# Performance work log

Hardware: AMD Instinct MI355X
Metric: run time of the kernel (lower is better)

## Reference

```python
import jax, jax.numpy as jnp
import numpy as np

K = 20  # max_similar_relations


def setup_inputs() -> dict:
    key = jax.random.key(0)
    k1, k2 = jax.random.split(key)
    B, R, D = 256, 2048, 64
    x = jax.random.normal(k1, (B, R, D), dtype=jnp.float32)
    query_rels = jax.random.randint(k2, (B,), 0, R, dtype=jnp.int32)
    return {
        "x": x,
        "query_rels": query_rels,
        # raw params as in __init__: threshold_init=0.2 -> raw=0.2*2-1=-0.6; strength_init=0.05 -> raw=0.05*5-1=-0.75
        "threshold_raw": jnp.float32(-0.6),
        "strength_raw": jnp.float32(-0.75),
        "weight_scale": jnp.float32(1.0),
        "temperature": jnp.float32(1.0),
    }


def reference(x, query_rels, threshold_raw, strength_raw, weight_scale, temperature):
    B, R, D = x.shape
    bidx = jnp.arange(B)
    threshold = jax.nn.sigmoid(threshold_raw)
    strength = jax.nn.sigmoid(strength_raw) * 0.2
    temp = jnp.clip(temperature, 0.1, 10.0)

    # F.normalize(x, p=2, dim=2)
    norms = x / jnp.maximum(jnp.linalg.norm(x, axis=2, keepdims=True), 1e-12)

    q = norms[bidx, query_rels]                      # [B, D] normalized query reprs
    sims = jnp.einsum("bd,brd->br", q, norms)        # [B, R] cosine similarities
    sims = sims.at[bidx, query_rels].set(-1.0)       # exclude self
    sim_w = jax.nn.sigmoid((sims - threshold) * 10.0)

    topv, topi = jax.lax.top_k(sims, K)              # [B, K]
    valid = (topv > threshold) & (topi != query_rels[:, None])

    # softmax over valid top-k entries only (per batch row)
    logits = jnp.where(valid, topv / temp, -1e9)
    w = jax.nn.softmax(logits, axis=1)
    w = jnp.where(valid, w, 0.0)

    sw = jnp.take_along_axis(sim_w, topi, axis=1)    # smooth sigmoid weights of selected
    combined = w * sw
    adjusted = combined * (1.0 + weight_scale * topv)
    adjusted = adjusted / (jnp.sum(adjusted, axis=1, keepdims=True) + 1e-8)

    # gather top-k normalized reprs and weighted-sum them
    top_reprs = jnp.take_along_axis(norms, jnp.broadcast_to(topi[:, :, None], (B, K, D)), axis=1)
    weighted = jnp.einsum("bk,bkd->bd", adjusted, top_reprs)  # [B, D]

    q_orig = x[bidx, query_rels]                     # original (unnormalized) query repr
    has_valid = jnp.any(valid, axis=1, keepdims=True)
    mixed = (1.0 - strength) * q_orig + strength * weighted
    new_q = jnp.where(has_valid, mixed, q_orig)

    return x.at[bidx, query_rels].set(new_q)
```

## Files before the change

### kernel.cpp

```cpp
#include <hip/hip_runtime.h>
#include <math.h>

#define KTOP 20
#define R_MAX 2048

__global__ __launch_bounds__(1024) void fused_enhancer(
    const float* __restrict__ x,
    const int* __restrict__ qrels,
    const float* __restrict__ thr_raw,
    const float* __restrict__ str_raw,
    const float* __restrict__ wscale_p,
    const float* __restrict__ temp_p,
    float* __restrict__ out, int R)
{
    __shared__ float s_q[64];
    __shared__ float s_sims[R_MAX];
    __shared__ float s_dn[R_MAX];
    __shared__ int   s_cand[R_MAX];
    __shared__ int   s_ncand;
    __shared__ float s_topv[KTOP];
    __shared__ int   s_topi[KTOP];
    __shared__ float s_adj[KTOP];
    __shared__ float s_strength;

    const int b = blockIdx.x;
    const int t = threadIdx.x;
    const int qr = qrels[b];
    const float threshold = 1.0f / (1.0f + expf(-thr_raw[0]));

    if (t == 0) s_ncand = 0;

    if (t < 64) {
        float v = x[((long)b * R + qr) * 64 + t];
        float ss = v * v;
#pragma unroll
        for (int m = 1; m < 64; m <<= 1) ss += __shfl_xor(ss, m, 64);
        s_q[t] = v / fmaxf(sqrtf(ss), 1e-12f);
    }
    __syncthreads();

    const int grp = t >> 4, l16 = t & 15;
    const float4 q4 = *(const float4*)(s_q + l16 * 4);
    const long xbase = (long)b * R * 64;
    for (int row = grp; row < R; row += 64) {
        long base = xbase + (long)row * 64 + l16 * 4;
        const float4 v = *(const float4*)(x + base);
        *(float4*)(out + base) = v;
        float dot = v.x * q4.x + v.y * q4.y + v.z * q4.z + v.w * q4.w;
        float ss  = v.x * v.x + v.y * v.y + v.z * v.z + v.w * v.w;
#pragma unroll
        for (int m = 1; m < 16; m <<= 1) {
            dot += __shfl_xor(dot, m, 64);
            ss  += __shfl_xor(ss,  m, 64);
        }
        if (l16 == 0) {
            float dn  = fmaxf(sqrtf(ss), 1e-12f);
            float sim = (row == qr) ? -1.0f : dot / dn;
            s_sims[row] = sim;
            s_dn[row]   = dn;
            if (sim > threshold) {
                int p = atomicAdd(&s_ncand, 1);
                s_cand[p] = row;
            }
        }
    }
    __syncthreads();

    const int ncand = s_ncand;
    const int ksel = ncand < KTOP ? ncand : KTOP;

    if (t < 64) {
        if (ncand > KTOP) {
            float lv[32]; int li[32];
#pragma unroll
            for (int j = 0; j < 32; ++j) {
                int i = t + 64 * j;
                if (i < ncand) { li[j] = s_cand[i]; lv[j] = s_sims[li[j]]; }
                else           { li[j] = 0x7fffffff; lv[j] = -INFINITY; }
            }
            for (int k = 0; k < KTOP; ++k) {
                float bv = -INFINITY; int bi = 0x7fffffff;
#pragma unroll
                for (int j = 0; j < 32; ++j) {
                    if (lv[j] > bv || (lv[j] == bv && li[j] < bi)) { bv = lv[j]; bi = li[j]; }
                }
#pragma unroll
                for (int m = 1; m < 64; m <<= 1) {
                    float v2 = __shfl_xor(bv, m, 64);
                    int   i2 = __shfl_xor(bi, m, 64);
                    if (v2 > bv || (v2 == bv && i2 < bi)) { bv = v2; bi = i2; }
                }
#pragma unroll
                for (int j = 0; j < 32; ++j) if (li[j] == bi) lv[j] = -INFINITY;
                if (t == 0) { s_topv[k] = bv; s_topi[k] = bi; }
            }
        } else if (t == 0) {
            for (int k = 0; k < ksel; ++k) {
                int idx = s_cand[k];
                s_topi[k] = idx;
                s_topv[k] = s_sims[idx];
            }
        }
    }

    if (t == 0) {
        float strength = (1.0f / (1.0f + expf(-str_raw[0]))) * 0.2f;
        float temp = fminf(fmaxf(temp_p[0], 0.1f), 10.0f);
        float wsc  = wscale_p[0];
        if (ksel > 0) {
            float m = -INFINITY;
            for (int k = 0; k < ksel; ++k) m = fmaxf(m, s_topv[k] / temp);
            float w[KTOP]; float wsum = 0.0f;
            for (int k = 0; k < ksel; ++k) { w[k] = expf(s_topv[k] / temp - m); wsum += w[k]; }
            float adj[KTOP]; float asum = 0.0f;
            for (int k = 0; k < ksel; ++k) {
                float tv = s_topv[k];
                float sw = 1.0f / (1.0f + expf(-(tv - threshold) * 10.0f));
                float a  = (w[k] / wsum) * sw * (1.0f + wsc * tv);
                adj[k] = a; asum += a;
            }
            for (int k = 0; k < ksel; ++k)
                s_adj[k] = (adj[k] / (asum + 1e-8f)) / s_dn[s_topi[k]];
        }
        s_strength = strength;
    }
    __syncthreads();

    if (t < 64 && ksel > 0) {
        long qb = ((long)b * R + qr) * 64 + t;
        float qo = x[qb];
        float acc = 0.0f;
        for (int k = 0; k < ksel; ++k)
            acc += s_adj[k] * x[((long)b * R + s_topi[k]) * 64 + t];
        float st = s_strength;
        out[qb] = (1.0f - st) * qo + st * acc;
    }
}

extern "C" void kernel_launch(void* const* d_in, const int* in_sizes, int n_in,
                              void* d_out, int out_size, void* d_ws, size_t ws_size,
                              hipStream_t stream) {
    const float* x      = (const float*)d_in[0];
    const int*   qrels  = (const int*)d_in[1];
    const float* thr    = (const float*)d_in[2];
    const float* str    = (const float*)d_in[3];
    const float* wscale = (const float*)d_in[4];
    const float* temp   = (const float*)d_in[5];
    float* out = (float*)d_out;

    const int B = in_sizes[1];
    const int D = 64;
    const int R = in_sizes[0] / (B * D);
    (void)D; (void)d_ws; (void)ws_size;

    fused_enhancer<<<B, 1024, 0, stream>>>(x, qrels, thr, str, wscale, temp, out, R);
}
```

Measured before the change: 253.0 us.

## Split fused kernel into qnorm, parallel copy/sims, and select kernels

Replaces the single one-block-per-batch kernel with three kernels. A tiny kernel normalizes the query, a wide grid (R/128 × B blocks) streams the copy and computes similarities with nontemporal loads and stores, and a per-batch wave does the threshold filtering and top-k selection over sims stored in workspace. The aim is far more parallelism for the memory-bound copy, which with only 256 large blocks may not saturate bandwidth. The cost is extra launches and a round trip of sims and norms through global memory, and the select kernel now scans all R entries instead of a compact candidate list.

```diff
diff --git a/kernel.cpp b/kernel.cpp
--- a/kernel.cpp
+++ b/kernel.cpp
@@ -2,50 +2,43 @@
 #include <math.h>
 
 #define KTOP 20
-#define R_MAX 2048
+#define RPB 128
 
-__global__ __launch_bounds__(1024) void fused_enhancer(
-    const float* __restrict__ x,
-    const int* __restrict__ qrels,
-    const float* __restrict__ thr_raw,
-    const float* __restrict__ str_raw,
-    const float* __restrict__ wscale_p,
-    const float* __restrict__ temp_p,
-    float* __restrict__ out, int R)
+typedef float vfloat4 __attribute__((ext_vector_type(4)));
+
+__global__ __launch_bounds__(64) void qnorm_kernel(
+    const float* __restrict__ x, const int* __restrict__ qrels,
+    float* __restrict__ qn, int R)
 {
-    __shared__ float s_q[64];
-    __shared__ float s_sims[R_MAX];
-    __shared__ float s_dn[R_MAX];
-    __shared__ int   s_cand[R_MAX];
-    __shared__ int   s_ncand;
-    __shared__ float s_topv[KTOP];
-    __shared__ int   s_topi[KTOP];
-    __shared__ float s_adj[KTOP];
-    __shared__ float s_strength;
+    int b = blockIdx.x;
+    int t = threadIdx.x;
+    int qr = qrels[b];
+    float v = x[((long)b * R + qr) * 64 + t];
+    float ss = v * v;
+#pragma unroll
+    for (int m = 1; m < 64; m <<= 1) ss += __shfl_xor(ss, m, 64);
+    qn[b * 64 + t] = v / fmaxf(sqrtf(ss), 1e-12f);
+}
 
-    const int b = blockIdx.x;
+__global__ __launch_bounds__(256) void copy_sims_kernel(
+    const float* __restrict__ x, const int* __restrict__ qrels,
+    const float* __restrict__ qn, float* __restrict__ out,
+    float* __restrict__ sims, float* __restrict__ dnorm, int R)
+{
+    const int b = blockIdx.y;
     const int t = threadIdx.x;
+    const int grp = t >> 4, l16 = t & 15;
     const int qr = qrels[b];
-    const float threshold = 1.0f / (1.0f + expf(-thr_raw[0]));
+    const vfloat4 q4 = *(const vfloat4*)(qn + b * 64 + l16 * 4);
+    const long xbase = (long)b * R * 64;
+    const int row0 = blockIdx.x * RPB;
 
-    if (t == 0) s_ncand = 0;
-
-    if (t < 64) {
-        float v = x[((long)b * R + qr) * 64 + t];
-        float ss = v * v;
 #pragma unroll
-        for (int m = 1; m < 64; m <<= 1) ss += __shfl_xor(ss, m, 64);
-        s_q[t] = v / fmaxf(sqrtf(ss), 1e-12f);
-    }
-    __syncthreads();
-
-    const int grp = t >> 4, l16 = t & 15;
-    const float4 q4 = *(const float4*)(s_q + l16 * 4);
-    const long xbase = (long)b * R * 64;
-    for (int row = grp; row < R; row += 64) {
+    for (int i = 0; i < RPB / 16; ++i) {
+        int row = row0 + i * 16 + grp;
         long base = xbase + (long)row * 64 + l16 * 4;
-        const float4 v = *(const float4*)(x + base);
-        *(float4*)(out + base) = v;
+        const vfloat4 v = __builtin_nontemporal_load((const vfloat4*)(x + base));
+        __builtin_nontemporal_store(v, (vfloat4*)(out + base));
         float dot = v.x * q4.x + v.y * q4.y + v.z * q4.z + v.w * q4.w;
         float ss  = v.x * v.x + v.y * v.y + v.z * v.z + v.w * v.w;
 #pragma unroll
@@ -54,79 +47,83 @@
             ss  += __shfl_xor(ss,  m, 64);
         }
         if (l16 == 0) {
-            float dn  = fmaxf(sqrtf(ss), 1e-12f);
-            float sim = (row == qr) ? -1.0f : dot / dn;
-            s_sims[row] = sim;
-            s_dn[row]   = dn;
-            if (sim > threshold) {
-                int p = atomicAdd(&s_ncand, 1);
-                s_cand[p] = row;
-            }
+            float dn = fmaxf(sqrtf(ss), 1e-12f);
+            sims[(long)b * R + row]  = (row == qr) ? -1.0f : dot / dn;
+            dnorm[(long)b * R + row] = dn;
         }
+    }
+}
+
+__global__ __launch_bounds__(64) void select_kernel(
+    const float* __restrict__ x, const int* __restrict__ qrels,
+    const float* __restrict__ sims, const float* __restrict__ dnorm,
+    const float* __restrict__ thr_raw, const float* __restrict__ str_raw,
+    const float* __restrict__ wscale_p, const float* __restrict__ temp_p,
+    float* __restrict__ out, int R)
+{
+    __shared__ float s_topv[KTOP];
+    __shared__ int   s_topi[KTOP];
+    __shared__ float s_adj[KTOP];
+    __shared__ float s_strength;
+
+    const int b = blockIdx.x;
+    const int t = threadIdx.x;
+    const float threshold = 1.0f / (1.0f + expf(-thr_raw[0]));
+
+    float lv[32]; int li[32];
+#pragma unroll
+    for (int j = 0; j < 32; ++j) {
+        int r = t + 64 * j;
+        if (r < R) {
+            float s = sims[(long)b * R + r];
+            lv[j] = (s > threshold) ? s : -INFINITY;
+            li[j] = r;
+        } else { lv[j] = -INFINITY; li[j] = 0x7fffffff; }
+    }
+
+    int ksel = 0;
+    for (int k = 0; k < KTOP; ++k) {
+        float bv = -INFINITY; int bi = 0x7fffffff;
+#pragma unroll
+        for (int j = 0; j < 32; ++j) {
+            if (lv[j] > bv) { bv = lv[j]; bi = li[j]; }
+        }
+#pragma unroll
+        for (int m = 1; m < 64; m <<= 1) {
+            float v2 = __shfl_xor(bv, m, 64);
+            int   i2 = __shfl_xor(bi, m, 64);
+            if (v2 > bv || (v2 == bv && i2 < bi)) { bv = v2; bi = i2; }
+        }
+        if (bv == -INFINITY) break;
+        if (t == 0) { s_topv[k] = bv; s_topi[k] = bi; }
+        ++ksel;
+#pragma unroll
+        for (int j = 0; j < 32; ++j) if (li[j] == bi) lv[j] = -INFINITY;
     }
     __syncthreads();
 
-    const int ncand = s_ncand;
-    const int ksel = ncand < KTOP ? ncand : KTOP;
-
-    if (t < 64) {
-        if (ncand > KTOP) {
-            float lv[32]; int li[32];
-#pragma unroll
-            for (int j = 0; j < 32; ++j) {
-                int i = t + 64 * j;
-                if (i < ncand) { li[j] = s_cand[i]; lv[j] = s_sims[li[j]]; }
-                else           { li[j] = 0x7fffffff; lv[j] = -INFINITY; }
-            }
-            for (int k = 0; k < KTOP; ++k) {
-                float bv = -INFINITY; int bi = 0x7fffffff;
-#pragma unroll
-                for (int j = 0; j < 32; ++j) {
-                    if (lv[j] > bv || (lv[j] == bv && li[j] < bi)) { bv = lv[j]; bi = li[j]; }
-                }
-#pragma unroll
-                for (int m = 1; m < 64; m <<= 1) {
-                    float v2 = __shfl_xor(bv, m, 64);
-                    int   i2 = __shfl_xor(bi, m, 64);
-                    if (v2 > bv || (v2 == bv && i2 < bi)) { bv = v2; bi = i2; }
-                }
-#pragma unroll
-                for (int j = 0; j < 32; ++j) if (li[j] == bi) lv[j] = -INFINITY;
-                if (t == 0) { s_topv[k] = bv; s_topi[k] = bi; }
-            }
-        } else if (t == 0) {
-            for (int k = 0; k < ksel; ++k) {
-                int idx = s_cand[k];
-                s_topi[k] = idx;
-                s_topv[k] = s_sims[idx];
-            }
-        }
-    }
-
-    if (t == 0) {
-        float strength = (1.0f / (1.0f + expf(-str_raw[0]))) * 0.2f;
+    if (t == 0 && ksel > 0) {
         float temp = fminf(fmaxf(temp_p[0], 0.1f), 10.0f);
         float wsc  = wscale_p[0];
-        if (ksel > 0) {
-            float m = -INFINITY;
-            for (int k = 0; k < ksel; ++k) m = fmaxf(m, s_topv[k] / temp);
-            float w[KTOP]; float wsum = 0.0f;
-            for (int k = 0; k < ksel; ++k) { w[k] = expf(s_topv[k] / temp - m); wsum += w[k]; }
-            float adj[KTOP]; float asum = 0.0f;
-            for (int k = 0; k < ksel; ++k) {
-                float tv = s_topv[k];
-                float sw = 1.0f / (1.0f + expf(-(tv - threshold) * 10.0f));
-                float a  = (w[k] / wsum) * sw * (1.0f + wsc * tv);
-                adj[k] = a; asum += a;
-            }
-            for (int k = 0; k < ksel; ++k)
-                s_adj[k] = (adj[k] / (asum + 1e-8f)) / s_dn[s_topi[k]];
+        float m = -INFINITY;
+        for (int k = 0; k < ksel; ++k) m = fmaxf(m, s_topv[k] / temp);
+        float w[KTOP]; float wsum = 0.0f;
+        for (int k = 0; k < ksel; ++k) { w[k] = expf(s_topv[k] / temp - m); wsum += w[k]; }
+        float adj[KTOP]; float asum = 0.0f;
+        for (int k = 0; k < ksel; ++k) {
+            float tv = s_topv[k];
+            float sw = 1.0f / (1.0f + expf(-(tv - threshold) * 10.0f));
+            float a  = (w[k] / wsum) * sw * (1.0f + wsc * tv);
+            adj[k] = a; asum += a;
         }
-        s_strength = strength;
+        for (int k = 0; k < ksel; ++k)
+            s_adj[k] = (adj[k] / (asum + 1e-8f)) / dnorm[(long)b * R + s_topi[k]];
+        s_strength = (1.0f / (1.0f + expf(-str_raw[0]))) * 0.2f;
     }
     __syncthreads();
 
-    if (t < 64 && ksel > 0) {
+    if (ksel > 0) {
+        const int qr = qrels[b];
         long qb = ((long)b * R + qr) * 64 + t;
         float qo = x[qb];
         float acc = 0.0f;
@@ -151,7 +148,17 @@
     const int B = in_sizes[1];
     const int D = 64;
     const int R = in_sizes[0] / (B * D);
-    (void)D; (void)d_ws; (void)ws_size;
+    (void)D; (void)ws_size;
 
-    fused_enhancer<<<B, 1024, 0, stream>>>(x, qrels, thr, str, wscale, temp, out, R);
+    float* qn    = (float*)d_ws;
+    float* sims  = qn + (size_t)B * 64;
+    float* dnorm = sims + (size_t)B * R;
+
+    qnorm_kernel<<<B, 64, 0, stream>>>(x, qrels, qn, R);
+
+    dim3 grid2(R / RPB, B);
+    copy_sims_kernel<<<grid2, 256, 0, stream>>>(x, qrels, qn, out, sims, dnorm, R);
+
+    select_kernel<<<B, 64, 0, stream>>>(x, qrels, sims, dnorm,
+                                        thr, str, wscale, temp, out, R);
 }
```

After: 262.6 us. +3.8%, slower.
